# Performance work log

Hardware: AMD Instinct MI355X
Metric: run time of the kernel (lower is better)

The kernel has to match this reference:

```python
import jax, jax.numpy as jnp
import numpy as np

B, N, C, H = 16, 577, 768, 12
KEEP_RATE = 0.7


def setup_inputs() -> dict:
    key = jax.random.key(0)
    k1, k2, k3 = jax.random.split(key, 3)
    x = jax.random.normal(k1, (B, N, C), dtype=jnp.float32)
    W_qkv = jax.random.normal(k2, (C, 3 * C), dtype=jnp.float32) * 0.02
    W_proj = jax.random.normal(k3, (C, C), dtype=jnp.float32) * 0.02
    b_proj = jnp.zeros((C,), dtype=jnp.float32)
    return {"x": x, "W_qkv": W_qkv, "W_proj": W_proj, "b_proj": b_proj}


def reference(x, W_qkv, W_proj, b_proj):
    b, n, c = x.shape
    h = H
    dh = c // h
    scale = dh ** (-0.5)

    # qkv projection -> q,k,v each [B,H,N,dh]
    qkv = (x @ W_qkv).reshape(b, n, 3, h, dh)
    qkv = jnp.transpose(qkv, (2, 0, 3, 1, 4))
    q, k, v = qkv[0], qkv[1], qkv[2]

    # full attention scores [B,H,N,N] (materialized, as in the source)
    attn = jnp.einsum('bhnd,bhmd->bhnm', q, k) * scale

    # --- top_pool from row-0 (CLS) scores, attn_method == 'SUM_ABS_1' ---
    # attn[:, :, 0, :] -> [B,H,N]; sum |.| over heads -> [B,N] (== mean over C=1 channel)
    attn_weight = jnp.sum(jnp.abs(attn[:, :, 0, :]), axis=1)  # [B,N]
    # exclude_first=True: drop CLS, topk over remaining N-1, alpha1=1, alpha2=0 (C==1 -> std=0)
    w = attn_weight[:, 1:]                       # [B, N-1]
    keep_num = max(int((n - 1) * KEEP_RATE), 1)  # static
    _, idx = jax.lax.top_k(w, keep_num)          # [B, keep_num]
    idx = jnp.sort(idx, axis=1)
    idx = jnp.concatenate(
        [jnp.zeros((b, 1), dtype=idx.dtype), idx + 1], axis=1)  # prepend CLS index 0
    # expand to [B, keep_num+1, dim] as in torch (pool dim kwarg == self.dim)
    keep_index = jnp.broadcast_to(idx[:, :, None], (b, keep_num + 1, c))

    # standard attention output
    a = jax.nn.softmax(attn, axis=-1)
    out = jnp.einsum('bhnm,bhmd->bhnd', a, v)    # [B,H,N,dh]
    out = jnp.transpose(out, (0, 2, 1, 3)).reshape(b, n, c)
    out = out @ W_proj + b_proj
    return out, keep_index
```

## Files before the change

### kernel.cpp

```cpp
#include <hip/hip_runtime.h>
#include <hip/hip_bf16.h>
#include <stdint.h>

#define B_    16
#define N_    577
#define C_    768
#define H_    12
#define M_    (B_*N_)
#define QKVN  (3*C_)
#define NKEEP 403
#define KROWS (NKEEP+1)
#define VTLD  640
#define PTLD  72

typedef short s16x8 __attribute__((ext_vector_type(8)));
typedef float f32x4 __attribute__((ext_vector_type(4)));

__device__ __forceinline__ unsigned short f2bf(float x){
  unsigned int u = __float_as_uint(x);
  u += 0x7FFF + ((u >> 16) & 1);
  return (unsigned short)(u >> 16);
}

__device__ __forceinline__ void gld_lds16(const void* g, void* l){
  __builtin_amdgcn_global_load_lds(
      (const __attribute__((address_space(1))) unsigned int*)g,
      (__attribute__((address_space(3))) unsigned int*)l, 16, 0, 0);
}

template<int NT, int M9, int MTILES>
__device__ __forceinline__ void tile_map(int L, int& mt, int& nt){
  constexpr int NB = MTILES*NT;
  int x = L & 7, j = L >> 3;
  if(j < M9*NT){
    nt = j/M9; mt = x*M9 + (j - nt*M9);
  } else {
    int offt = 0;
    #pragma unroll
    for(int y=0;y<8;y++) if(y<x) offt += ((NB-1-y)>>3) + 1 - M9*NT;
    int ft = offt + (j - M9*NT);
    mt = 8*M9 + ft/NT;
    nt = ft - (ft/NT)*NT;
  }
}

__global__ void k_cvt_x(const float* __restrict__ x, unsigned short* __restrict__ xb){
  int i = blockIdx.x*256 + threadIdx.x;
  float4 v = ((const float4*)x)[i];
  ushort4 o; o.x=f2bf(v.x); o.y=f2bf(v.y); o.z=f2bf(v.z); o.w=f2bf(v.w);
  ((ushort4*)xb)[i] = o;
}

__global__ void k_transpose_cvt(const float* __restrict__ in, unsigned short* __restrict__ out,
                                int R, int CC){
  __shared__ float tile[64][65];
  int r0 = blockIdx.y*64, c0 = blockIdx.x*64;
  int tx = threadIdx.x & 63, ty = threadIdx.x >> 6;
  #pragma unroll
  for(int i=0;i<16;i++){
    int r = ty + i*4;
    tile[r][tx] = in[(size_t)(r0+r)*CC + c0 + tx];
  }
  __syncthreads();
  #pragma unroll
  for(int i=0;i<16;i++){
    int c = ty + i*4;
    out[(size_t)(c0+c)*R + r0 + tx] = f2bf(tile[tx][c]);
  }
}

template<int LDC_, bool BF16OUT, bool FUSEV, int NT>
__global__ __launch_bounds__(256) void k_gemm_bt(const unsigned short* __restrict__ A,
                          const unsigned short* __restrict__ Bt,
                          void* __restrict__ Cout,
                          const float* __restrict__ bias, int Mdim,
                          unsigned short* __restrict__ vtbuf){
  __shared__ __align__(16) unsigned short As[128*32];
  __shared__ __align__(16) unsigned short Bs[128*32];
  const int t = threadIdx.x;
  const int w = t>>6, l = t&63, lq = l>>4, lr = l&15;
  const int wm = w>>1, wn = w&1;
  int mt, nt; tile_map<NT, 9, 73>(blockIdx.x, mt, nt);
  const int m0 = mt*128, n0 = nt*128;
  int rA0 = m0 + (t>>2);       if(rA0 >= Mdim) rA0 = Mdim-1;
  int rA1 = m0 + ((t+256)>>2); if(rA1 >= Mdim) rA1 = Mdim-1;
  const unsigned short* gA0 = A  + (size_t)rA0*768 + (t&3)*8;
  const unsigned short* gA1 = A  + (size_t)rA1*768 + (t&3)*8;
  const unsigned short* gB0 = Bt + (size_t)(n0 + (t>>2))*768 + (t&3)*8;
  const unsigned short* gB1 = Bt + (size_t)(n0 + ((t+256)>>2))*768 + (t&3)*8;
  unsigned short* lA0 = As + (size_t)w*512;
  unsigned short* lA1 = As + 2048 + (size_t)w*512;
  unsigned short* lB0 = Bs + (size_t)w*512;
  unsigned short* lB1 = Bs + 2048 + (size_t)w*512;
  f32x4 acc[4][4] = {};
  for(int kt=0; kt<24; ++kt){
    const int ko = kt*32;
    __syncthreads();
    gld_lds16(gA0 + ko, lA0); gld_lds16(gA1 + ko, lA1);
    gld_lds16(gB0 + ko, lB0); gld_lds16(gB1 + ko, lB1);
    __syncthreads();
    s16x8 af[4], bfr[4];
    #pragma unroll
    for(int it=0;it<4;it++) af[it]  = *(const s16x8*)&As[(wm*64+it*16+lr)*32 + lq*8];
    #pragma unroll
    for(int jt=0;jt<4;jt++) bfr[jt] = *(const s16x8*)&Bs[(wn*64+jt*16+lr)*32 + lq*8];
    #pragma unroll
    for(int it=0;it<4;it++)
      #pragma unroll
      for(int jt=0;jt<4;jt++)
        acc[it][jt] = __builtin_amdgcn_mfma_f32_16x16x32_bf16(af[it], bfr[jt], acc[it][jt], 0,0,0);
  }
  if(FUSEV && n0 >= 1536){
    #pragma unroll
    for(int it=0;it<4;it++){
      int tok0 = m0 + wm*64 + it*16 + lq*4;
      #pragma unroll
      for(int jt=0;jt<4;jt++){
        int vrow = (n0 - 1536) + wn*64 + jt*16 + lr;
        ushort4 pk; unsigned short* pks = (unsigned short*)&pk;
        #pragma unroll
        for(int r=0;r<4;r++) pks[r] = f2bf(acc[it][jt][r]);
        int b0 = tok0/577, t0 = tok0 - b0*577;
        if(tok0 + 3 < M_ && t0 + 3 < 577){
          *(ushort4*)&vtbuf[(size_t)(b0*768 + vrow)*VTLD + t0] = pk;
        } else {
          #pragma unroll
          for(int r=0;r<4;r++){
            int tg = tok0 + r;
            if(tg < M_){
              int bb = tg/577, tt = tg - bb*577;
              vtbuf[(size_t)(bb*768 + vrow)*VTLD + tt] = pks[r];
            }
          }
        }
      }
    }
  } else {
    #pragma unroll
    for(int it=0;it<4;it++){
      #pragma unroll
      for(int r=0;r<4;r++){
        int row = m0 + wm*64 + it*16 + lq*4 + r;
        if(row < Mdim){
          #pragma unroll
          for(int jt=0;jt<4;jt++){
            int col = n0 + wn*64 + jt*16 + lr;
            float v = acc[it][jt][r];
            if constexpr (BF16OUT)
              ((unsigned short*)Cout)[(size_t)row*LDC_ + col] = f2bf(v);
            else
              ((float*)Cout)[(size_t)row*LDC_ + col] = v + bias[col];
          }
        }
      }
    }
  }
}

__global__ __launch_bounds__(256) void k_gemm_bt64(const unsigned short* __restrict__ A,
                          const unsigned short* __restrict__ Bt,
                          float* __restrict__ Cout,
                          const float* __restrict__ bias, int Mdim){
  __shared__ __align__(16) unsigned short As[64*32];
  __shared__ __align__(16) unsigned short Bs[128*32];
  const int t = threadIdx.x;
  const int w = t>>6, l = t&63, lq = l>>4, lr = l&15;
  const int wm = w>>1, wn = w&1;
  int mt, nt; tile_map<6, 18, 145>(blockIdx.x, mt, nt);
  const int m0 = mt*64, n0 = nt*128;
  int rA0 = m0 + (t>>2);       if(rA0 >= Mdim) rA0 = Mdim-1;
  const unsigned short* gA0 = A  + (size_t)rA0*768 + (t&3)*8;
  const unsigned short* gB0 = Bt + (size_t)(n0 + (t>>2))*768 + (t&3)*8;
  const unsigned short* gB1 = Bt + (size_t)(n0 + ((t+256)>>2))*768 + (t&3)*8;
  unsigned short* lA0 = As + (size_t)w*512;
  unsigned short* lB0 = Bs + (size_t)w*512;
  unsigned short* lB1 = Bs + 2048 + (size_t)w*512;
  f32x4 acc[2][4] = {};
  for(int kt=0; kt<24; ++kt){
    const int ko = kt*32;
    __syncthreads();
    gld_lds16(gA0 + ko, lA0);
    gld_lds16(gB0 + ko, lB0); gld_lds16(gB1 + ko, lB1);
    __syncthreads();
    s16x8 af[2], bfr[4];
    #pragma unroll
    for(int it=0;it<2;it++) af[it]  = *(const s16x8*)&As[(wm*32+it*16+lr)*32 + lq*8];
    #pragma unroll
    for(int jt=0;jt<4;jt++) bfr[jt] = *(const s16x8*)&Bs[(wn*64+jt*16+lr)*32 + lq*8];
    #pragma unroll
    for(int it=0;it<2;it++)
      #pragma unroll
      for(int jt=0;jt<4;jt++)
        acc[it][jt] = __builtin_amdgcn_mfma_f32_16x16x32_bf16(af[it], bfr[jt], acc[it][jt], 0,0,0);
  }
  #pragma unroll
  for(int it=0;it<2;it++){
    #pragma unroll
    for(int r=0;r<4;r++){
      int row = m0 + wm*32 + it*16 + lq*4 + r;
      if(row < Mdim){
        #pragma unroll
        for(int jt=0;jt<4;jt++){
          int col = n0 + wn*64 + jt*16 + lr;
          Cout[(size_t)row*768 + col] = acc[it][jt][r] + bias[col];
        }
      }
    }
  }
}

__global__ __launch_bounds__(256,4) void k_attn(const unsigned short* __restrict__ qkv,
                                                const unsigned short* __restrict__ vtbuf,
                                                unsigned short* __restrict__ aout){
  __shared__ __align__(16) unsigned short Ks[64*64];
  __shared__ __align__(16) unsigned short Vt[64*64];
  __shared__ __align__(16) unsigned short Ptt[128*PTLD];
  __shared__ float Ls[4][2][16][4];
  const int blk = blockIdx.x;
  const int bh = blk % 192, qt = blk / 192;
  const int b = bh / 12, h = bh % 12;
  const int t = threadIdx.x, w = t>>6, l = t&63, lq = l>>4, lr = l&15;
  const size_t base = (size_t)(b*577)*2304 + h*64;
  const int q0 = qt*128;
  s16x8 bq[2][2];
  #pragma unroll
  for(int it=0;it<2;it++){
    int qrow = q0 + w*32 + it*16 + lr; if(qrow > 576) qrow = 576;
    #pragma unroll
    for(int ks=0;ks<2;ks++)
      bq[it][ks] = *(const s16x8*)&qkv[base + (size_t)qrow*2304 + ks*32 + lq*8];
  }
  const int srow = w*8 + (l>>3);
  const int cswz8 = (((l&7) ^ (l>>3)) << 3);
  unsigned short* ldsK = Ks + w*512 + l*8;
  unsigned short* ldsV = Vt + w*512 + l*8;
  const unsigned short* gVbase = vtbuf + (size_t)(bh*64)*VTLD + cswz8;

  f32x4 acc_o[2][4] = {};
  float lsum[2] = {0.f, 0.f};
  const float CEXP = 0.18033688011112043f;

  s16x8 kreg0, kreg1, vreg0, vreg1;
  auto stage_issue = [&](int tt){
    const int j0i = tt*64;
    int kr0 = j0i + srow;      if(kr0 > 576) kr0 = 576;
    int kr1 = j0i + 32 + srow; if(kr1 > 576) kr1 = 576;
    kreg0 = *(const s16x8*)(qkv + base + 768 + (size_t)kr0*2304 + cswz8);
    kreg1 = *(const s16x8*)(qkv + base + 768 + (size_t)kr1*2304 + cswz8);
    vreg0 = *(const s16x8*)(gVbase + (size_t)srow*VTLD + j0i);
    vreg1 = *(const s16x8*)(gVbase + (size_t)(32 + srow)*VTLD + j0i);
  };

  stage_issue(0);
  for(int g=0; g<10; ++g){
    const int j0 = g*64;
    const bool edge = (g == 9);
    *(s16x8*)(ldsK)        = kreg0;
    *(s16x8*)(ldsK + 2048) = kreg1;
    *(s16x8*)(ldsV)        = vreg0;
    *(s16x8*)(ldsV + 2048) = vreg1;
    asm volatile("s_waitcnt lgkmcnt(0)" ::: "memory");
    __builtin_amdgcn_s_barrier();
    __builtin_amdgcn_sched_barrier(0);
    if(g < 9) stage_issue(g+1);

    f32x4 accs[2][4] = {};
    #pragma unroll
    for(int ks=0;ks<2;ks++){
      s16x8 ak[4];
      #pragma unroll
      for(int jt=0;jt<4;jt++){
        int j = jt*16 + lr;
        ak[jt] = *(const s16x8*)&Ks[j*64 + (((4*ks+lq) ^ (j&7))<<3)];
      }
      #pragma unroll
      for(int it=0;it<2;it++)
        #pragma unroll
        for(int jt=0;jt<4;jt++)
          accs[it][jt] = __builtin_amdgcn_mfma_f32_16x16x32_bf16(ak[jt], bq[it][ks], accs[it][jt], 0,0,0);
    }
    #pragma unroll
    for(int it=0;it<2;it++){
      int qlocal = w*32 + it*16 + lr;
      #pragma unroll
      for(int jt=0;jt<4;jt++){
        ushort4 pk;
        unsigned short* pks = (unsigned short*)&pk;
        #pragma unroll
        for(int r=0;r<4;r++){
          float p = exp2f(accs[it][jt][r] * CEXP);
          if(edge){ if(j0 + jt*16 + lq*4 + r > 576) p = 0.f; }
          lsum[it] += p;
          pks[r] = f2bf(p);
        }
        *(ushort4*)&Ptt[qlocal*PTLD + jt*16 + lq*4] = pk;
      }
    }
    #pragma unroll
    for(int ks=0;ks<2;ks++){
      s16x8 ap[2], bv[4];
      #pragma unroll
      for(int it=0;it<2;it++)
        ap[it] = *(const s16x8*)&Ptt[(w*32+it*16+lr)*PTLD + ks*32 + lq*8];
      #pragma unroll
      for(int dt=0;dt<4;dt++){
        int d = dt*16 + lr;
        bv[dt] = *(const s16x8*)&Vt[d*64 + (((4*ks+lq) ^ (d&7))<<3)];
      }
      #pragma unroll
      for(int it=0;it<2;it++)
        #pragma unroll
        for(int dt=0;dt<4;dt++)
          acc_o[it][dt] = __builtin_amdgcn_mfma_f32_16x16x32_bf16(ap[it], bv[dt], acc_o[it][dt], 0,0,0);
    }
    asm volatile("s_waitcnt lgkmcnt(0)" ::: "memory");
    __builtin_amdgcn_s_barrier();
    __builtin_amdgcn_sched_barrier(0);
  }

  #pragma unroll
  for(int it=0;it<2;it++) Ls[w][it][lr][lq] = lsum[it];
  #pragma unroll
  for(int it=0;it<2;it++){
    #pragma unroll
    for(int r=0;r<4;r++){
      int n = q0 + w*32 + it*16 + lq*4 + r;
      if(n <= 576){
        int q16 = lq*4 + r;
        float lt = Ls[w][it][q16][0] + Ls[w][it][q16][1] + Ls[w][it][q16][2] + Ls[w][it][q16][3];
        float inv = 1.f / lt;
        #pragma unroll
        for(int dt=0;dt<4;dt++)
          aout[(size_t)(b*577+n)*768 + h*64 + dt*16 + lr] = f2bf(acc_o[it][dt][r]*inv);
      }
    }
  }
}

__global__ void k_qcls(const float* __restrict__ x, const float* __restrict__ Wqkv,
                       float* __restrict__ qcls){
  __shared__ float xs[768];
  __shared__ float part[4][64];
  const int b = blockIdx.y, j0 = blockIdx.x*64;
  const int t = threadIdx.x;
  const float* xr = x + (size_t)b*577*768;
  xs[t] = xr[t]; xs[t+256] = xr[t+256]; xs[t+512] = xr[t+512];
  __syncthreads();
  const int jl = t & 63, cs = t >> 6;
  float acc = 0.f;
  const float* wp = Wqkv + (size_t)(cs*192)*2304 + j0 + jl;
  #pragma unroll 4
  for(int c=0;c<192;c++){ acc += xs[cs*192+c] * wp[0]; wp += 2304; }
  part[cs][jl] = acc;
  __syncthreads();
  if(t < 64) qcls[b*768 + j0 + t] = part[0][t]+part[1][t]+part[2][t]+part[3][t];
}
__global__ void k_u(const float* __restrict__ Wqkv, const float* __restrict__ qcls,
                    float* __restrict__ u){
  int h = blockIdx.x, b = blockIdx.y, c = threadIdx.x;
  const float* qc = qcls + b*768 + h*64;
  const float* wr = Wqkv + (size_t)c*2304 + 768 + h*64;
  float acc = 0.f;
  #pragma unroll
  for(int d=0;d<64;d++) acc += wr[d]*qc[d];
  u[(size_t)(b*12+h)*768 + c] = acc;
}
__global__ void k_attw(const float* __restrict__ x, const float* __restrict__ u,
                       float* __restrict__ attw){
  int blk = blockIdx.x;
  int b = blk/577, m = blk%577;
  int lane = threadIdx.x;
  const float* xr = x + (size_t)(b*577+m)*768;
  const float* ub = u + (size_t)b*12*768;
  float part[12];
  #pragma unroll
  for(int h=0;h<12;h++) part[h]=0.f;
  #pragma unroll
  for(int i=0;i<12;i++){
    float xv = xr[i*64 + lane];
    #pragma unroll
    for(int h=0;h<12;h++) part[h] += xv * ub[h*768 + i*64 + lane];
  }
  float s = 0.f;
  #pragma unroll
  for(int h=0;h<12;h++){
    float v = part[h];
    #pragma unroll
    for(int off=32; off; off>>=1) v += __shfl_xor(v, off);
    s += fabsf(v);
  }
  if(lane==0) attw[b*577 + m] = 0.125f * s;
}
__global__ void k_topk(const float* __restrict__ attw, int* __restrict__ idxbuf){
  __shared__ float sw[576];
  __shared__ int wtot[9];
  int b = blockIdx.x, t = threadIdx.x;
  float wv = attw[b*577 + 1 + t];
  sw[t] = wv;
  __syncthreads();
  int rank = 0;
  for(int j=0;j<576;j++){
    float wj = sw[j];
    rank += (wj > wv) || (wj == wv && j < t);
  }
  bool kept = rank < NKEEP;
  unsigned long long mask = __ballot(kept);
  int wid = t>>6, lane = t&63;
  int pos = __popcll(mask & ((1ull<<lane)-1ull));
  if(lane==0) wtot[wid] = __popcll(mask);
  __syncthreads();
  int off0 = 0;
  for(int q=0;q<wid;q++) off0 += wtot[q];
  if(kept) idxbuf[b*KROWS + 1 + off0 + pos] = t+1;
  if(t==0) idxbuf[b*KROWS] = 0;
}
__global__ void k_fill_keep(const int* __restrict__ idxbuf, float* __restrict__ out2){
  int i4 = blockIdx.x*256 + threadIdx.x;
  float v = (float)idxbuf[i4/192];
  ((float4*)out2)[i4] = make_float4(v,v,v,v);
}

extern "C" void kernel_launch(void* const* d_in, const int* in_sizes, int n_in,
                              void* d_out, int out_size, void* d_ws, size_t ws_size,
                              hipStream_t stream){
  const float* x     = (const float*)d_in[0];
  const float* Wqkv  = (const float*)d_in[1];
  const float* Wproj = (const float*)d_in[2];
  const float* bias  = (const float*)d_in[3];
  float* out  = (float*)d_out;
  float* out2 = out + (size_t)M_*768;

  char* ws = (char*)d_ws;
  size_t off = 0;
  auto alloc = [&](size_t bytes)->void*{ void* p = ws + off; off += (bytes + 255) & ~(size_t)255; return p; };
  unsigned short* xb     = (unsigned short*)alloc((size_t)M_*768*2);
  unsigned short* wqkvT  = (unsigned short*)alloc((size_t)QKVN*768*2);
  unsigned short* wprojT = (unsigned short*)alloc((size_t)768*768*2);
  unsigned short* qkvb   = (unsigned short*)alloc((size_t)M_*QKVN*2);
  unsigned short* aoutb  = (unsigned short*)alloc((size_t)M_*768*2);
  unsigned short* vtbuf  = (unsigned short*)alloc((size_t)192*64*VTLD*2);
  float* qcls   = (float*)alloc((size_t)16*768*4);
  float* u      = (float*)alloc((size_t)16*12*768*4);
  float* attw   = (float*)alloc((size_t)16*577*4);
  int*   idxbuf = (int*)alloc((size_t)16*KROWS*4);

  k_cvt_x<<<6924, 256, 0, stream>>>(x, xb);
  k_transpose_cvt<<<dim3(36,12), 256, 0, stream>>>(Wqkv,  wqkvT, 768, 2304);
  k_transpose_cvt<<<dim3(12,12), 256, 0, stream>>>(Wproj, wprojT, 768, 768);
  k_gemm_bt<QKVN, true, true, 18><<<73*18, 256, 0, stream>>>(xb, wqkvT, qkvb, nullptr, M_, vtbuf);
  k_qcls<<<dim3(12,16), 256, 0, stream>>>(x, Wqkv, qcls);
  k_u<<<dim3(12,16), 768, 0, stream>>>(Wqkv, qcls, u);
  k_attw<<<16*577, 64, 0, stream>>>(x, u, attw);
  k_topk<<<16, 576, 0, stream>>>(attw, idxbuf);
  k_fill_keep<<<(16*KROWS*768/4 + 255)/256, 256, 0, stream>>>(idxbuf, out2);
  k_attn<<<960, 256, 0, stream>>>(qkvb, vtbuf, aoutb);
  k_gemm_bt64<<<145*6, 256, 0, stream>>>(aoutb, wprojT, out, bias, M_);
}
```

Measured before the change: 281.4 us.

## Fuse prep kernels, add K64 swizzled QKV GEMM, merge topk with fill

Folds the x conversion, both weight transposes and the CLS-query projection into one prep launch. The QKV projection moves to a new GEMM that stages 64-wide K slices with an XOR-swizzled LDS layout and a 128x128 tile, halving the number of K iterations and barriers. Top-k now writes the keep-index output directly from shared memory, and the output projection switches to the 128-row tile GEMM. This cuts launch count and sync overhead, at the cost of larger LDS use per block, and the 16-block fill kernel has less parallelism than the old standalone fill.

```diff
diff --git a/kernel.cpp b/kernel.cpp
--- a/kernel.cpp
+++ b/kernel.cpp
@@ -44,28 +44,50 @@
   }
 }
 
-__global__ void k_cvt_x(const float* __restrict__ x, unsigned short* __restrict__ xb){
-  int i = blockIdx.x*256 + threadIdx.x;
-  float4 v = ((const float4*)x)[i];
-  ushort4 o; o.x=f2bf(v.x); o.y=f2bf(v.y); o.z=f2bf(v.z); o.w=f2bf(v.w);
-  ((ushort4*)xb)[i] = o;
-}
-
-__global__ void k_transpose_cvt(const float* __restrict__ in, unsigned short* __restrict__ out,
-                                int R, int CC){
+__global__ __launch_bounds__(256) void k_prep(const float* __restrict__ x,
+                       const float* __restrict__ Wqkv, const float* __restrict__ Wproj,
+                       unsigned short* __restrict__ xb, unsigned short* __restrict__ wqkvT,
+                       unsigned short* __restrict__ wprojT, float* __restrict__ qcls){
   __shared__ float tile[64][65];
-  int r0 = blockIdx.y*64, c0 = blockIdx.x*64;
-  int tx = threadIdx.x & 63, ty = threadIdx.x >> 6;
-  #pragma unroll
-  for(int i=0;i<16;i++){
-    int r = ty + i*4;
-    tile[r][tx] = in[(size_t)(r0+r)*CC + c0 + tx];
-  }
-  __syncthreads();
-  #pragma unroll
-  for(int i=0;i<16;i++){
-    int c = ty + i*4;
-    out[(size_t)(c0+c)*R + r0 + tx] = f2bf(tile[tx][c]);
+  __shared__ float part[4][64];
+  const int bid = blockIdx.x, t = threadIdx.x;
+  if(bid < 6924){
+    int i = bid*256 + t;
+    float4 v = ((const float4*)x)[i];
+    ushort4 o; o.x=f2bf(v.x); o.y=f2bf(v.y); o.z=f2bf(v.z); o.w=f2bf(v.w);
+    ((ushort4*)xb)[i] = o;
+  } else if(bid < 7500){
+    const float* in; unsigned short* out; int R, CC, bx, by;
+    if(bid < 7356){ int r = bid - 6924; bx = r % 36; by = r / 36; in = Wqkv;  out = wqkvT;  R = 768; CC = 2304; }
+    else          { int r = bid - 7356; bx = r % 12; by = r / 12; in = Wproj; out = wprojT; R = 768; CC = 768;  }
+    int r0 = by*64, c0 = bx*64;
+    int tx = t & 63, ty = t >> 6;
+    #pragma unroll
+    for(int i=0;i<16;i++){
+      int r = ty + i*4;
+      tile[r][tx] = in[(size_t)(r0+r)*CC + c0 + tx];
+    }
+    __syncthreads();
+    #pragma unroll
+    for(int i=0;i<16;i++){
+      int c = ty + i*4;
+      out[(size_t)(c0+c)*R + r0 + tx] = f2bf(tile[tx][c]);
+    }
+  } else {
+    int r = bid - 7500;
+    const int b = r / 12, j0 = (r % 12)*64;
+    float* xs = &tile[0][0];
+    const float* xr = x + (size_t)b*577*768;
+    xs[t] = xr[t]; xs[t+256] = xr[t+256]; xs[t+512] = xr[t+512];
+    __syncthreads();
+    const int jl = t & 63, cs = t >> 6;
+    float acc = 0.f;
+    const float* wp = Wqkv + (size_t)(cs*192)*2304 + j0 + jl;
+    #pragma unroll 4
+    for(int c=0;c<192;c++){ acc += xs[cs*192+c] * wp[0]; wp += 2304; }
+    part[cs][jl] = acc;
+    __syncthreads();
+    if(t < 64) qcls[b*768 + j0 + t] = part[0][t]+part[1][t]+part[2][t]+part[3][t];
   }
 }
 
@@ -157,52 +179,97 @@
   }
 }
 
-__global__ __launch_bounds__(256) void k_gemm_bt64(const unsigned short* __restrict__ A,
+template<int LDC_, bool BF16OUT, bool FUSEV, int NT>
+__global__ __launch_bounds__(256) void k_gemm_bt_k64(const unsigned short* __restrict__ A,
                           const unsigned short* __restrict__ Bt,
-                          float* __restrict__ Cout,
-                          const float* __restrict__ bias, int Mdim){
-  __shared__ __align__(16) unsigned short As[64*32];
-  __shared__ __align__(16) unsigned short Bs[128*32];
+                          void* __restrict__ Cout,
+                          const float* __restrict__ bias, int Mdim,
+                          unsigned short* __restrict__ vtbuf){
+  __shared__ __align__(16) unsigned short As[128*64];
+  __shared__ __align__(16) unsigned short Bs[128*64];
   const int t = threadIdx.x;
   const int w = t>>6, l = t&63, lq = l>>4, lr = l&15;
   const int wm = w>>1, wn = w&1;
-  int mt, nt; tile_map<6, 18, 145>(blockIdx.x, mt, nt);
-  const int m0 = mt*64, n0 = nt*128;
-  int rA0 = m0 + (t>>2);       if(rA0 >= Mdim) rA0 = Mdim-1;
-  const unsigned short* gA0 = A  + (size_t)rA0*768 + (t&3)*8;
-  const unsigned short* gB0 = Bt + (size_t)(n0 + (t>>2))*768 + (t&3)*8;
-  const unsigned short* gB1 = Bt + (size_t)(n0 + ((t+256)>>2))*768 + (t&3)*8;
-  unsigned short* lA0 = As + (size_t)w*512;
-  unsigned short* lB0 = Bs + (size_t)w*512;
-  unsigned short* lB1 = Bs + 2048 + (size_t)w*512;
-  f32x4 acc[2][4] = {};
-  for(int kt=0; kt<24; ++kt){
-    const int ko = kt*32;
-    __syncthreads();
-    gld_lds16(gA0 + ko, lA0);
-    gld_lds16(gB0 + ko, lB0); gld_lds16(gB1 + ko, lB1);
-    __syncthreads();
-    s16x8 af[2], bfr[4];
-    #pragma unroll
-    for(int it=0;it<2;it++) af[it]  = *(const s16x8*)&As[(wm*32+it*16+lr)*32 + lq*8];
-    #pragma unroll
-    for(int jt=0;jt<4;jt++) bfr[jt] = *(const s16x8*)&Bs[(wn*64+jt*16+lr)*32 + lq*8];
-    #pragma unroll
-    for(int it=0;it<2;it++)
-      #pragma unroll
-      for(int jt=0;jt<4;jt++)
-        acc[it][jt] = __builtin_amdgcn_mfma_f32_16x16x32_bf16(af[it], bfr[jt], acc[it][jt], 0,0,0);
-  }
-  #pragma unroll
-  for(int it=0;it<2;it++){
-    #pragma unroll
-    for(int r=0;r<4;r++){
-      int row = m0 + wm*32 + it*16 + lq*4 + r;
-      if(row < Mdim){
-        #pragma unroll
-        for(int jt=0;jt<4;jt++){
-          int col = n0 + wn*64 + jt*16 + lr;
-          Cout[(size_t)row*768 + col] = acc[it][jt][r] + bias[col];
+  int mt, nt; tile_map<NT, 9, 73>(blockIdx.x, mt, nt);
+  const int m0 = mt*128, n0 = nt*128;
+  const int srow = t>>3;
+  const int csw  = (((t&7) ^ ((t>>3)&7))<<3);
+  const unsigned short* gA[4]; const unsigned short* gB[4];
+  #pragma unroll
+  for(int i=0;i<4;i++){
+    int ra = m0 + i*32 + srow; if(ra >= Mdim) ra = Mdim-1;
+    gA[i] = A  + (size_t)ra*768 + csw;
+    gB[i] = Bt + (size_t)(n0 + i*32 + srow)*768 + csw;
+  }
+  unsigned short* dA = As + (size_t)w*512;
+  unsigned short* dB = Bs + (size_t)w*512;
+  const int rxa = lr&7;
+  f32x4 acc[4][4] = {};
+  for(int kt=0; kt<12; ++kt){
+    const int ko = kt*64;
+    __syncthreads();
+    #pragma unroll
+    for(int i=0;i<4;i++){
+      gld_lds16(gA[i] + ko, dA + i*2048);
+      gld_lds16(gB[i] + ko, dB + i*2048);
+    }
+    __syncthreads();
+    #pragma unroll
+    for(int ks=0;ks<2;ks++){
+      s16x8 af[4], bfr[4];
+      const int cx = ((ks*4 + lq) ^ rxa) << 3;
+      #pragma unroll
+      for(int it=0;it<4;it++) af[it]  = *(const s16x8*)&As[(wm*64+it*16+lr)*64 + cx];
+      #pragma unroll
+      for(int jt=0;jt<4;jt++) bfr[jt] = *(const s16x8*)&Bs[(wn*64+jt*16+lr)*64 + cx];
+      #pragma unroll
+      for(int it=0;it<4;it++)
+        #pragma unroll
+        for(int jt=0;jt<4;jt++)
+          acc[it][jt] = __builtin_amdgcn_mfma_f32_16x16x32_bf16(af[it], bfr[jt], acc[it][jt], 0,0,0);
+    }
+  }
+  if(FUSEV && n0 >= 1536){
+    #pragma unroll
+    for(int it=0;it<4;it++){
+      int tok0 = m0 + wm*64 + it*16 + lq*4;
+      #pragma unroll
+      for(int jt=0;jt<4;jt++){
+        int vrow = (n0 - 1536) + wn*64 + jt*16 + lr;
+        ushort4 pk; unsigned short* pks = (unsigned short*)&pk;
+        #pragma unroll
+        for(int r=0;r<4;r++) pks[r] = f2bf(acc[it][jt][r]);
+        int b0 = tok0/577, t0 = tok0 - b0*577;
+        if(tok0 + 3 < M_ && t0 + 3 < 577){
+          *(ushort4*)&vtbuf[(size_t)(b0*768 + vrow)*VTLD + t0] = pk;
+        } else {
+          #pragma unroll
+          for(int r=0;r<4;r++){
+            int tg = tok0 + r;
+            if(tg < M_){
+              int bb = tg/577, tt = tg - bb*577;
+              vtbuf[(size_t)(bb*768 + vrow)*VTLD + tt] = pks[r];
+            }
+          }
+        }
+      }
+    }
+  } else {
+    #pragma unroll
+    for(int it=0;it<4;it++){
+      #pragma unroll
+      for(int r=0;r<4;r++){
+        int row = m0 + wm*64 + it*16 + lq*4 + r;
+        if(row < Mdim){
+          #pragma unroll
+          for(int jt=0;jt<4;jt++){
+            int col = n0 + wn*64 + jt*16 + lr;
+            float v = acc[it][jt][r];
+            if constexpr (BF16OUT)
+              ((unsigned short*)Cout)[(size_t)row*LDC_ + col] = f2bf(v);
+            else
+              ((float*)Cout)[(size_t)row*LDC_ + col] = v + bias[col];
+          }
         }
       }
     }
@@ -337,24 +404,6 @@
   }
 }
 
-__global__ void k_qcls(const float* __restrict__ x, const float* __restrict__ Wqkv,
-                       float* __restrict__ qcls){
-  __shared__ float xs[768];
-  __shared__ float part[4][64];
-  const int b = blockIdx.y, j0 = blockIdx.x*64;
-  const int t = threadIdx.x;
-  const float* xr = x + (size_t)b*577*768;
-  xs[t] = xr[t]; xs[t+256] = xr[t+256]; xs[t+512] = xr[t+512];
-  __syncthreads();
-  const int jl = t & 63, cs = t >> 6;
-  float acc = 0.f;
-  const float* wp = Wqkv + (size_t)(cs*192)*2304 + j0 + jl;
-  #pragma unroll 4
-  for(int c=0;c<192;c++){ acc += xs[cs*192+c] * wp[0]; wp += 2304; }
-  part[cs][jl] = acc;
-  __syncthreads();
-  if(t < 64) qcls[b*768 + j0 + t] = part[0][t]+part[1][t]+part[2][t]+part[3][t];
-}
 __global__ void k_u(const float* __restrict__ Wqkv, const float* __restrict__ qcls,
                     float* __restrict__ u){
   int h = blockIdx.x, b = blockIdx.y, c = threadIdx.x;
@@ -391,9 +440,10 @@
   }
   if(lane==0) attw[b*577 + m] = 0.125f * s;
 }
-__global__ void k_topk(const float* __restrict__ attw, int* __restrict__ idxbuf){
+__global__ void k_topk_fill(const float* __restrict__ attw, float* __restrict__ out2){
   __shared__ float sw[576];
   __shared__ int wtot[9];
+  __shared__ int sidx[KROWS];
   int b = blockIdx.x, t = threadIdx.x;
   float wv = attw[b*577 + 1 + t];
   sw[t] = wv;
@@ -411,13 +461,14 @@
   __syncthreads();
   int off0 = 0;
   for(int q=0;q<wid;q++) off0 += wtot[q];
-  if(kept) idxbuf[b*KROWS + 1 + off0 + pos] = t+1;
-  if(t==0) idxbuf[b*KROWS] = 0;
-}
-__global__ void k_fill_keep(const int* __restrict__ idxbuf, float* __restrict__ out2){
-  int i4 = blockIdx.x*256 + threadIdx.x;
-  float v = (float)idxbuf[i4/192];
-  ((float4*)out2)[i4] = make_float4(v,v,v,v);
+  if(kept) sidx[1 + off0 + pos] = t+1;
+  if(t==0) sidx[0] = 0;
+  __syncthreads();
+  float4* o4 = (float4*)out2 + (size_t)b*KROWS*192;
+  for(int i = t; i < KROWS*192; i += 576){
+    float v = (float)sidx[i/192];
+    o4[i] = make_float4(v,v,v,v);
+  }
 }
 
 extern "C" void kernel_launch(void* const* d_in, const int* in_sizes, int n_in,
@@ -442,17 +493,12 @@
   float* qcls   = (float*)alloc((size_t)16*768*4);
   float* u      = (float*)alloc((size_t)16*12*768*4);
   float* attw   = (float*)alloc((size_t)16*577*4);
-  int*   idxbuf = (int*)alloc((size_t)16*KROWS*4);
-
-  k_cvt_x<<<6924, 256, 0, stream>>>(x, xb);
-  k_transpose_cvt<<<dim3(36,12), 256, 0, stream>>>(Wqkv,  wqkvT, 768, 2304);
-  k_transpose_cvt<<<dim3(12,12), 256, 0, stream>>>(Wproj, wprojT, 768, 768);
-  k_gemm_bt<QKVN, true, true, 18><<<73*18, 256, 0, stream>>>(xb, wqkvT, qkvb, nullptr, M_, vtbuf);
-  k_qcls<<<dim3(12,16), 256, 0, stream>>>(x, Wqkv, qcls);
+
+  k_prep<<<7692, 256, 0, stream>>>(x, Wqkv, Wproj, xb, wqkvT, wprojT, qcls);
+  k_gemm_bt_k64<QKVN, true, true, 18><<<73*18, 256, 0, stream>>>(xb, wqkvT, qkvb, nullptr, M_, vtbuf);
   k_u<<<dim3(12,16), 768, 0, stream>>>(Wqkv, qcls, u);
   k_attw<<<16*577, 64, 0, stream>>>(x, u, attw);
-  k_topk<<<16, 576, 0, stream>>>(attw, idxbuf);
-  k_fill_keep<<<(16*KROWS*768/4 + 255)/256, 256, 0, stream>>>(idxbuf, out2);
+  k_topk_fill<<<16, 576, 0, stream>>>(attw, out2);
   k_attn<<<960, 256, 0, stream>>>(qkvb, vtbuf, aoutb);
-  k_gemm_bt64<<<145*6, 256, 0, stream>>>(aoutb, wprojT, out, bias, M_);
-}
+  k_gemm_bt<768, false, false, 6><<<73*6, 256, 0, stream>>>(aoutb, wprojT, out, bias, M_, nullptr);
+}
```

After: 271.5 us. -3.5%, faster.
